# Performance work log

Measured on AMD Instinct MI355X. Metric: run time of the kernel, lower is better.

## Reference

```python
import jax, jax.numpy as jnp
import numpy as np

B, DIM, H, W = 2, 192, 256, 256
WIN = 4
EPS = 1e-5


def _cd_conj(x):
    if len(x) == 1:
        return x
    h = len(x) // 2
    return np.concatenate([_cd_conj(x[:h]), -x[h:]])


def _cd_mult(a, b):
    n = len(a)
    if n == 1:
        return a * b
    h = n // 2
    a1, a2, b1, b2 = a[:h], a[h:], b[:h], b[h:]
    c1 = _cd_mult(a1, b1) - _cd_mult(_cd_conj(b2), a2)
    c2 = _cd_mult(b2, a1) + _cd_mult(a2, _cd_conj(b1))
    return np.concatenate([c1, c2])


def _sedenion_table(n=16):
    # M[i, j, k] = sign s such that e_i * e_j = s * e_k (Cayley-Dickson)
    eye = np.eye(n, dtype=np.float32)
    M = np.zeros((n, n, n), dtype=np.float32)
    for i in range(n):
        for j in range(n):
            M[i, j] = _cd_mult(eye[i], eye[j])
    return M

SED_TABLE = jnp.asarray(_sedenion_table(16))  # (16,16,16)


def layer_norm(x, g, b):
    m = x.mean(-1, keepdims=True)
    v = ((x - m) ** 2).mean(-1, keepdims=True)
    return (x - m) * jax.lax.rsqrt(v + EPS) * g + b


def get_window(x):
    # (B,C,H,W) -> (B,H/4,W/4, s1*s2*C)
    b, c, h, w = x.shape
    x = x.reshape(b, c, h // WIN, WIN, w // WIN, WIN)
    x = x.transpose(0, 2, 4, 3, 5, 1)  # b, h', w', s1, s2, c
    return x.reshape(b, h // WIN, w // WIN, WIN * WIN * c)


def reverse_window(x, c):
    b, hh, ww, _ = x.shape
    x = x.reshape(b, hh, ww, WIN, WIN, c)
    x = x.transpose(0, 5, 1, 3, 2, 4)  # b, c, h', s1, w', s2
    return x.reshape(b, c, hh * WIN, ww * WIN)


def sedenion_full_weight(w_sed):
    # w_sed: (16, dim, dim) component weights -> (16*dim, 16*dim) structured matrix
    d = w_sed.shape[1]
    wf = jnp.einsum('ijk,jde->idke', SED_TABLE, w_sed)
    return wf.reshape(16 * d, 16 * w_sed.shape[2])


def setup_inputs() -> dict:
    key = jax.random.key(0)
    ks = jax.random.split(key, 8)
    d, dh = DIM, 4 * DIM
    s = 0.02
    return {
        'x': jax.random.normal(ks[0], (B, DIM, H, W), jnp.float32),
        'norm1_g': jnp.ones((d,), jnp.float32),
        'norm1_b': jnp.zeros((d,), jnp.float32),
        'w_sed': jax.random.normal(ks[1], (16, d, d), jnp.float32) * s,
        'proj_w': jax.random.normal(ks[2], (d, d), jnp.float32) * s,
        'proj_b': jnp.zeros((d,), jnp.float32),
        'norm2_g': jnp.ones((d,), jnp.float32),
        'norm2_b': jnp.zeros((d,), jnp.float32),
        'fc1_w': jax.random.normal(ks[3], (d, dh), jnp.float32) * s,
        'fc1_b': jnp.zeros((dh,), jnp.float32),
        'fc2_w': jax.random.normal(ks[4], (dh, d), jnp.float32) * s,
        'fc2_b': jnp.zeros((d,), jnp.float32),
    }


def reference(x, norm1_g, norm1_b, w_sed, proj_w, proj_b,
              norm2_g, norm2_b, fc1_w, fc1_b, fc2_w, fc2_b):
    b, c, h, w = x.shape
    # --- attention branch (norm1 -> window -> sedenion linear -> unwindow -> gelu -> proj) ---
    xn = layer_norm(x.transpose(0, 2, 3, 1), norm1_g, norm1_b).transpose(0, 3, 1, 2)
    xw = get_window(xn)                               # (B, H/4, W/4, 16*C)
    wf = sedenion_full_weight(w_sed)                  # (16C, 16C)
    xw = xw @ wf
    x1 = reverse_window(xw, c)                        # (B, C, H, W)
    y = x1.transpose(0, 2, 3, 1)                      # b h w c
    y = jax.nn.gelu(y, approximate=False)
    y = y @ proj_w + proj_b
    x = x + y.transpose(0, 3, 1, 2)
    # --- mlp branch ---
    hbr = layer_norm(x.transpose(0, 2, 3, 1), norm2_g, norm2_b)
    hbr = jax.nn.gelu(hbr @ fc1_w + fc1_b, approximate=False)
    hbr = hbr @ fc2_w + fc2_b
    x = x + hbr.transpose(0, 3, 1, 2)
    return x
```

## Files before the change

kernel.cpp:

```cpp
#include <hip/hip_runtime.h>

typedef short short8 __attribute__((ext_vector_type(8)));
typedef float f32x4 __attribute__((ext_vector_type(4)));

#define DEVINL __device__ __forceinline__

struct SedTab { signed char s[256]; unsigned char j[256]; };

static void cd_mult_host(const float* a, const float* b, float* r, int n) {
    if (n == 1) { r[0] = a[0] * b[0]; return; }
    int h = n / 2;
    float cb1[8], cb2[8], t1[8], t2[8], t3[8], t4[8];
    cb1[0] = b[0]; for (int i = 1; i < h; ++i) cb1[i] = -b[i];
    cb2[0] = b[h]; for (int i = 1; i < h; ++i) cb2[i] = -b[h + i];
    cd_mult_host(a,     b,   t1, h);
    cd_mult_host(cb2,   a+h, t2, h);
    cd_mult_host(b+h,   a,   t3, h);
    cd_mult_host(a+h,   cb1, t4, h);
    for (int i = 0; i < h; ++i) { r[i] = t1[i] - t2[i]; r[h + i] = t3[i] + t4[i]; }
}

static SedTab build_sed() {
    SedTab t{};
    for (int i = 0; i < 16; ++i)
        for (int jj = 0; jj < 16; ++jj) {
            float a[16] = {0}, b[16] = {0}, r[16] = {0};
            a[i] = 1.0f; b[jj] = 1.0f;
            cd_mult_host(a, b, r, 16);
            for (int k = 0; k < 16; ++k)
                if (r[k] != 0.0f) {
                    t.s[i * 16 + k] = (r[k] > 0.f) ? 1 : -1;
                    t.j[i * 16 + k] = (unsigned char)jj;
                }
        }
    return t;
}
static const SedTab g_sed = build_sed();

DEVINL unsigned short f2bf(float v) {
    union { float f; unsigned int u; } c; c.f = v;
    unsigned int r = (c.u + 0x7FFFu + ((c.u >> 16) & 1u)) >> 16;
    return (unsigned short)r;
}
DEVINL float bf2f(unsigned short u) {
    union { unsigned int i; float f; } c; c.i = ((unsigned int)u) << 16; return c.f;
}

DEVINL float gelu_f(float v) {
    float u = 1.5957691216f * (v + 0.044715f * v * v * v);
    return v / (1.0f + __expf(-u));
}

DEVINL void gl2lds16(const void* g, void* l) {
    __builtin_amdgcn_global_load_lds((__attribute__((address_space(1))) const unsigned int*)g,
                                     (__attribute__((address_space(3))) unsigned int*)l, 16, 0, 0);
}

DEVINL int swz(int k, int row) {
    return (k & ~63) | ((((k >> 3) ^ row) & 7) << 3) | (k & 7);
}

__global__ __launch_bounds__(256) void build_wft(const float* __restrict__ w_sed,
                                                 unsigned short* __restrict__ wfT,
                                                 SedTab tab) {
    __shared__ float t[32][33];
    int n0 = blockIdx.y * 32, kk0 = blockIdx.x * 32;
    int k = n0 / 192, i = kk0 / 192;
    int j = tab.j[i * 16 + k];
    float s = (float)tab.s[i * 16 + k];
    int e0 = n0 - k * 192, dd0 = kk0 - i * 192;
    int tx = threadIdx.x & 31, ty = threadIdx.x >> 5;
    const float* base = w_sed + ((size_t)j * 192 + dd0) * 192 + e0;
    for (int it = 0; it < 4; ++it) {
        int row = ty + it * 8;
        t[row][tx] = base[(size_t)row * 192 + tx];
    }
    __syncthreads();
    unsigned short* ob = wfT + (size_t)n0 * 3072 + kk0;
    for (int it = 0; it < 4; ++it) {
        int row = ty + it * 8;
        ob[(size_t)row * 3072 + tx] = f2bf(s * t[tx][row]);
    }
}

__global__ __launch_bounds__(256) void prep_w(const float* __restrict__ proj,
                                              const float* __restrict__ fc1,
                                              const float* __restrict__ fc2,
                                              unsigned short* __restrict__ projT,
                                              unsigned short* __restrict__ fc1T,
                                              unsigned short* __restrict__ fc2T) {
    int t = blockIdx.x * 256 + threadIdx.x;
    if (t < 192 * 192) projT[t] = f2bf(proj[(t % 192) * 192 + t / 192]);
    if (t < 768 * 192) {
        int n = t / 192, k = t % 192;
        fc1T[n * 192 + swz(k, n)] = f2bf(fc1[(size_t)k * 768 + n]);
    }
    if (t < 192 * 768) {
        int o = t / 768, k = t % 768;
        fc2T[o * 768 + swz(k, o)] = f2bf(fc2[(size_t)k * 192 + o]);
    }
}

__global__ __launch_bounds__(256) void ln1_win(const float* __restrict__ x,
                                               const float* __restrict__ g,
                                               const float* __restrict__ bta,
                                               unsigned short* __restrict__ xw,
                                               unsigned short* __restrict__ xwin) {
    __shared__ float vals[192 * 65];
    __shared__ float ps[8][64];
    __shared__ float mrs[2][64];
    int t = threadIdx.x;
    int bid = blockIdx.x;
    int x0 = (bid & 3) << 6;
    int y  = (bid >> 2) & 255;
    int b  = bid >> 10;
    int px = t & 63, cg = t >> 6;
    const float* xp = x + ((size_t)b * 192 * 65536) + (size_t)y * 256 + x0 + px;
    float s = 0.f, s2 = 0.f;
    for (int c = cg; c < 192; c += 4) {
        float v = xp[(size_t)c * 65536];
        vals[c * 65 + px] = v;
        s += v; s2 += v * v;
    }
    ps[cg][px] = s; ps[cg + 4][px] = s2;
    __syncthreads();
    if (t < 64) {
        float S  = ps[0][t] + ps[1][t] + ps[2][t] + ps[3][t];
        float S2 = ps[4][t] + ps[5][t] + ps[6][t] + ps[7][t];
        float mean = S * (1.0f / 192.0f);
        float var  = S2 * (1.0f / 192.0f) - mean * mean;
        mrs[0][t] = mean;
        mrs[1][t] = rsqrtf(var + 1e-5f);
    }
    __syncthreads();
    int wh = y >> 2, wr = y & 3;
    for (int i = t; i < 192 * 64; i += 256) {
        int p = i / 192;
        int c = i - p * 192;
        float v = vals[c * 65 + p];
        int xx = x0 + p;
        int ww = xx >> 2, wc = xx & 3;
        int gp = ((b * 64 + wh) * 64 + ww) * 16 + wr * 4 + wc;
        size_t o = (size_t)gp * 192 + c;
        xwin[o] = f2bf(v);
        xw[o] = f2bf((v - mrs[0][p]) * mrs[1][p] * g[c] + bta[c]);
    }
}

template<int TM, int TN, int EPI>
__global__ __launch_bounds__(256, 2) void gemm_bf16(
        const unsigned short* __restrict__ A, const unsigned short* __restrict__ BT,
        const float* __restrict__ bias, unsigned short* __restrict__ outB,
        unsigned short* __restrict__ xresb,
        const float* __restrict__ g2, const float* __restrict__ b2,
        int K, int N) {
    constexpr int WN = TN / 2;
    constexpr int NT = WN / 16;
    constexpr int MT = TM / 32;
    constexpr int HR = TM / 2;
    __shared__ __align__(16) char smem[(TM * 64 + TN * 64) * 2];
    short* lsA = (short*)smem;
    short* lsB = (short*)(smem + TM * 64 * 2);
    int tid = threadIdx.x, lane = tid & 63, wid = tid >> 6;
    int wrow = wid >> 1, wcol = wid & 1;
    int lm = lane & 15, lq = lane >> 4;
    int bm = blockIdx.x * TM, bn = blockIdx.y * TN;
    const unsigned short* Ag = A + (size_t)bm * K;
    const unsigned short* Bg = BT + (size_t)bn * K;
    f32x4 acc[MT][NT] = {};
    for (int k0 = 0; k0 < K; k0 += 64) {
        #pragma unroll
        for (int it = 0; it < TM / 32; ++it) {
            int p = (it * 4 + wid) * 64 + lane;
            int r = p >> 3;
            int q = (p & 7) ^ (r & 7);
            gl2lds16(Ag + (size_t)r * K + k0 + q * 8, lsA + (it * 4 + wid) * 512);
        }
        #pragma unroll
        for (int it = 0; it < TN / 32; ++it) {
            int p = (it * 4 + wid) * 64 + lane;
            int r = p >> 3;
            int q = (p & 7) ^ (r & 7);
            gl2lds16(Bg + (size_t)r * K + k0 + q * 8, lsB + (it * 4 + wid) * 512);
        }
        __syncthreads();
        #pragma unroll
        for (int s = 0; s < 2; ++s) {
            short8 af[MT], bfr[NT];
            #pragma unroll
            for (int mt = 0; mt < MT; ++mt) {
                int r = wrow * HR + mt * 16 + lm;
                int q = s * 4 + lq;
                int pos = r * 8 + (q ^ (r & 7));
                af[mt] = *(const short8*)&lsA[pos * 8];
            }
            #pragma unroll
            for (int nt = 0; nt < NT; ++nt) {
                int r = wcol * WN + nt * 16 + lm;
                int q = s * 4 + lq;
                int pos = r * 8 + (q ^ (r & 7));
                bfr[nt] = *(const short8*)&lsB[pos * 8];
            }
            #pragma unroll
            for (int mt = 0; mt < MT; ++mt)
                #pragma unroll
                for (int nt = 0; nt < NT; ++nt)
                    acc[mt][nt] = __builtin_amdgcn_mfma_f32_16x16x32_bf16(af[mt], bfr[nt], acc[mt][nt], 0, 0, 0);
        }
        __syncthreads();
    }
    int rowB = bm + wrow * HR + lq * 4;
    int colB = bn + wcol * WN + lm;

    if constexpr (EPI == 0) {
        #pragma unroll
        for (int mt = 0; mt < MT; ++mt)
            #pragma unroll
            for (int nt = 0; nt < NT; ++nt)
                #pragma unroll
                for (int r = 0; r < 4; ++r) {
                    int gr = rowB + mt * 16 + r;
                    int gc = colB + nt * 16;
                    float v = acc[mt][nt][r];
                    if (bias) v += bias[gc];
                    outB[(size_t)gr * N + gc] = f2bf(gelu_f(v));
                }
    } else {
        float sA[MT][4], s2A[MT][4];
        #pragma unroll
        for (int mt = 0; mt < MT; ++mt)
            #pragma unroll
            for (int r = 0; r < 4; ++r) { sA[mt][r] = 0.f; s2A[mt][r] = 0.f; }
        #pragma unroll
        for (int mt = 0; mt < MT; ++mt)
            #pragma unroll
            for (int nt = 0; nt < NT; ++nt)
                #pragma unroll
                for (int r = 0; r < 4; ++r) {
                    int gr = rowB + mt * 16 + r;
                    int gc = colB + nt * 16;
                    size_t o = (size_t)gr * 192 + gc;
                    float v = bf2f(xresb[o]) + acc[mt][nt][r] + bias[gc];
                    xresb[o] = f2bf(v);
                    acc[mt][nt][r] = v;
                    sA[mt][r] += v; s2A[mt][r] += v * v;
                }
        #pragma unroll
        for (int mt = 0; mt < MT; ++mt)
            #pragma unroll
            for (int r = 0; r < 4; ++r)
                #pragma unroll
                for (int msk = 1; msk < 16; msk <<= 1) {
                    sA[mt][r]  += __shfl_xor(sA[mt][r],  msk, 64);
                    s2A[mt][r] += __shfl_xor(s2A[mt][r], msk, 64);
                }
        float* psS   = (float*)smem;
        float* psS2  = psS + 256;
        float* pmean = psS2 + 256;
        float* prsig = pmean + 128;
        if (lm == 0) {
            #pragma unroll
            for (int mt = 0; mt < MT; ++mt)
                #pragma unroll
                for (int r = 0; r < 4; ++r) {
                    int rl = wrow * HR + mt * 16 + lq * 4 + r;
                    psS [rl * 2 + wcol] = sA[mt][r];
                    psS2[rl * 2 + wcol] = s2A[mt][r];
                }
        }
        __syncthreads();
        if (tid < TM) {
            float S  = psS[tid * 2]  + psS[tid * 2 + 1];
            float S2 = psS2[tid * 2] + psS2[tid * 2 + 1];
            float mean = S * (1.0f / 192.0f);
            float var  = S2 * (1.0f / 192.0f) - mean * mean;
            pmean[tid] = mean;
            prsig[tid] = rsqrtf(var + 1e-5f);
        }
        __syncthreads();
        float gw[NT], bw[NT];
        #pragma unroll
        for (int nt = 0; nt < NT; ++nt) {
            int gc = colB + nt * 16;
            gw[nt] = g2[gc]; bw[nt] = b2[gc];
        }
        #pragma unroll
        for (int mt = 0; mt < MT; ++mt)
            #pragma unroll
            for (int nt = 0; nt < NT; ++nt)
                #pragma unroll
                for (int r = 0; r < 4; ++r) {
                    int gr = rowB + mt * 16 + r;
                    int rl = wrow * HR + mt * 16 + lq * 4 + r;
                    int gc = colB + nt * 16;
                    float v = (acc[mt][nt][r] - pmean[rl]) * prsig[rl] * gw[nt] + bw[nt];
                    outB[(size_t)gr * 192 + swz(gc, gr)] = f2bf(v);
                }
    }
}

__global__ __launch_bounds__(256, 2) void ffn_fused(
        const unsigned short* __restrict__ A3, const unsigned short* __restrict__ fc1T,
        const unsigned short* __restrict__ fc2T, const float* __restrict__ b1,
        const float* __restrict__ b2, const unsigned short* __restrict__ xresb,
        float* __restrict__ outF) {
    __shared__ __align__(16) char smem[81920];
    short* wA0 = (short*)smem;
    short* wA1 = (short*)(smem + 24576);
    short* wB  = (short*)(smem + 49152);
    short* Sb  = (short*)(smem + 73728);
    int tid = threadIdx.x, lane = tid & 63, wid = tid >> 6;
    int wrow = wid >> 1, wcol = wid & 1;
    int lm = lane & 15, lq = lane >> 4;
    int bm = blockIdx.x * 64;

    const unsigned short* A3g = A3 + (size_t)bm * 192;

    auto stage_fc1 = [&](int slice, short* dst) {
        const unsigned short* f1g = fc1T + (size_t)slice * 64 * 192;
        #pragma unroll
        for (int it = 0; it < 6; ++it) {
            int ch = (it * 4 + wid) * 64 + lane;
            gl2lds16(f1g + ch * 8, dst + (it * 4 + wid) * 512);
        }
    };
    auto stage_fc2 = [&](int slice) {
        int kb = slice * 64;
        #pragma unroll
        for (int it = 0; it < 6; ++it) {
            int ch = (it * 4 + wid) * 64 + lane;
            gl2lds16(fc2T + (size_t)(ch >> 3) * 768 + kb + (ch & 7) * 8,
                     wB + (it * 4 + wid) * 512);
        }
    };

    stage_fc1(0, wA0);
    stage_fc1(1, wA1);
    stage_fc2(0);

    short8 af[6][2];
    #pragma unroll
    for (int ks = 0; ks < 6; ++ks) {
        int c = ks * 4 + lq;
        #pragma unroll
        for (int mt = 0; mt < 2; ++mt) {
            int r = wrow * 32 + mt * 16 + lm;
            int slot = (c & ~7) | ((c ^ r) & 7);
            af[ks][mt] = *(const short8*)&A3g[(size_t)r * 192 + slot * 8];
        }
    }
    __syncthreads();

    f32x4 acc2[2][6] = {};
    for (int nb = 0; nb < 12; ++nb) {
        const short* wAc = (nb & 1) ? wA1 : wA0;
        f32x4 acc1[2][2] = {};
        __builtin_amdgcn_s_setprio(1);
        #pragma unroll
        for (int ks = 0; ks < 6; ++ks) {
            int c = ks * 4 + lq;
            short8 bfr[2];
            #pragma unroll
            for (int nt = 0; nt < 2; ++nt) {
                int n = wcol * 32 + nt * 16 + lm;
                int slot = (c & ~7) | ((c ^ n) & 7);
                bfr[nt] = *(const short8*)&wAc[n * 192 + slot * 8];
            }
            #pragma unroll
            for (int mt = 0; mt < 2; ++mt)
                #pragma unroll
                for (int nt = 0; nt < 2; ++nt)
                    acc1[mt][nt] = __builtin_amdgcn_mfma_f32_16x16x32_bf16(af[ks][mt], bfr[nt], acc1[mt][nt], 0, 0, 0);
        }
        __builtin_amdgcn_s_setprio(0);
        #pragma unroll
        for (int nt = 0; nt < 2; ++nt) {
            int cl = wcol * 32 + nt * 16 + lm;
            float bv = b1[nb * 64 + cl];
            #pragma unroll
            for (int mt = 0; mt < 2; ++mt)
                #pragma unroll
                for (int r = 0; r < 4; ++r) {
                    int row = wrow * 32 + mt * 16 + lq * 4 + r;
                    float v = gelu_f(acc1[mt][nt][r] + bv);
                    int slot = ((cl >> 3) ^ row) & 7;
                    Sb[row * 64 + slot * 8 + (cl & 7)] = f2bf(v);
                }
        }
        asm volatile("s_waitcnt vmcnt(0) lgkmcnt(0)" ::: "memory");
        __builtin_amdgcn_sched_barrier(0);
        __builtin_amdgcn_s_barrier();
        __builtin_amdgcn_sched_barrier(0);
        if (nb < 10) stage_fc1(nb + 2, (nb & 1) ? wA1 : wA0);
        __builtin_amdgcn_s_setprio(1);
        #pragma unroll
        for (int ks = 0; ks < 2; ++ks) {
            int c = ks * 4 + lq;
            short8 sf[2], wf[6];
            #pragma unroll
            for (int mt = 0; mt < 2; ++mt) {
                int r = wrow * 32 + mt * 16 + lm;
                int slot = (c ^ r) & 7;
                sf[mt] = *(const short8*)&Sb[r * 64 + slot * 8];
            }
            #pragma unroll
            for (int nt = 0; nt < 6; ++nt) {
                int o = wcol * 96 + nt * 16 + lm;
                int slot = (c ^ o) & 7;
                wf[nt] = *(const short8*)&wB[o * 64 + slot * 8];
            }
            #pragma unroll
            for (int mt = 0; mt < 2; ++mt)
                #pragma unroll
                for (int nt = 0; nt < 6; ++nt)
                    acc2[mt][nt] = __builtin_amdgcn_mfma_f32_16x16x32_bf16(sf[mt], wf[nt], acc2[mt][nt], 0, 0, 0);
        }
        __builtin_amdgcn_s_setprio(0);
        asm volatile("s_waitcnt lgkmcnt(0)" ::: "memory");
        __builtin_amdgcn_sched_barrier(0);
        __builtin_amdgcn_s_barrier();
        __builtin_amdgcn_sched_barrier(0);
        if (nb < 11) stage_fc2(nb + 1);
    }
    float* T = (float*)smem;
    #pragma unroll
    for (int nt = 0; nt < 6; ++nt) {
        int col = wcol * 96 + nt * 16 + lm;
        float bv = b2[col];
        #pragma unroll
        for (int mt = 0; mt < 2; ++mt)
            #pragma unroll
            for (int r = 0; r < 4; ++r) {
                int row = wrow * 32 + mt * 16 + lq * 4 + r;
                float xr = bf2f(xresb[(size_t)(bm + row) * 192 + col]);
                T[row * 201 + col] = acc2[mt][nt][r] + bv + xr;
            }
    }
    __syncthreads();
    int b  = bm >> 16;
    int wh = (bm >> 10) & 63;
    int ww0 = (bm >> 4) & 63;
    int ybase = wh * 4, xbase = ww0 * 4;
    for (int idx = tid; idx < 3072; idx += 256) {
        int xq = idx & 3, run = idx >> 2;
        int c = run >> 2, wr = run & 3;
        int p = xq * 16 + wr * 4;
        f32x4 val;
        val[0] = T[(p + 0) * 201 + c];
        val[1] = T[(p + 1) * 201 + c];
        val[2] = T[(p + 2) * 201 + c];
        val[3] = T[(p + 3) * 201 + c];
        size_t o = (((size_t)b * 192 + c) * 256 + (ybase + wr)) * 256 + xbase + xq * 4;
        *(f32x4*)&outF[o] = val;
    }
}

extern "C" void kernel_launch(void* const* d_in, const int* in_sizes, int n_in,
                              void* d_out, int out_size, void* d_ws, size_t ws_size,
                              hipStream_t stream) {
    const float* x      = (const float*)d_in[0];
    const float* n1g    = (const float*)d_in[1];
    const float* n1b    = (const float*)d_in[2];
    const float* w_sed  = (const float*)d_in[3];
    const float* proj_w = (const float*)d_in[4];
    const float* proj_b = (const float*)d_in[5];
    const float* n2g    = (const float*)d_in[6];
    const float* n2b    = (const float*)d_in[7];
    const float* fc1_w  = (const float*)d_in[8];
    const float* fc1_b  = (const float*)d_in[9];
    const float* fc2_w  = (const float*)d_in[10];
    const float* fc2_b  = (const float*)d_in[11];
    float* out = (float*)d_out;

    char* ws = (char*)d_ws;
    unsigned short* wfT   = (unsigned short*)(ws);
    unsigned short* xw    = (unsigned short*)(ws + 18874368);
    unsigned short* A2    = (unsigned short*)(ws + 69206016);
    unsigned short* xresb = (unsigned short*)(ws + 119537664);
    unsigned short* projT = (unsigned short*)(ws + 169869312);
    unsigned short* fc1T  = (unsigned short*)(ws + 169943040);
    unsigned short* fc2T  = (unsigned short*)(ws + 170237952);
    unsigned short* A3    = A2;

    build_wft<<<dim3(96, 96), 256, 0, stream>>>(w_sed, wfT, g_sed);
    prep_w<<<576, 256, 0, stream>>>(proj_w, fc1_w, fc2_w, projT, fc1T, fc2T);
    ln1_win<<<2048, 256, 0, stream>>>(x, n1g, n1b, xw, xresb);

    gemm_bf16<128, 128, 0><<<dim3(64, 24), 256, 0, stream>>>(
        xw, wfT, nullptr, A2, nullptr, nullptr, nullptr, 3072, 3072);
    gemm_bf16<128, 192, 3><<<dim3(1024, 1), 256, 0, stream>>>(
        A2, projT, proj_b, A3, xresb, n2g, n2b, 192, 192);
    ffn_fused<<<2048, 256, 0, stream>>>(A3, fc1T, fc2T, fc1_b, fc2_b, xresb, out);
}
```

Before: 582.3 us.

## Enlarge fused FFN blocks to 256 rows and write output directly from registers

The fused FFN kernel now runs 1024-thread blocks covering 256 rows instead of 64, so each block stages the fc1/fc2 weight slices once for four times as many rows. Weight staging is rewritten as one or two 16-byte loads per thread. The LDS transpose epilogue is dropped: each lane adds bias and the bf16 residual and stores an f32x4 straight to NCHW output. GELU uses a hardware reciprocal instead of a divide. The risks are that __launch_bounds__(1024,4) caps registers per thread hard enough to cause spills, and the larger LDS footprint lowers occupancy.

New measurement: 832.2 us. +42.9%, slower.

```diff
diff --git a/kernel.cpp b/kernel.cpp
--- a/kernel.cpp
+++ b/kernel.cpp
@@ -48,7 +48,7 @@
 
 DEVINL float gelu_f(float v) {
     float u = 1.5957691216f * (v + 0.044715f * v * v * v);
-    return v / (1.0f + __expf(-u));
+    return v * __builtin_amdgcn_rcpf(1.0f + __expf(-u));
 }
 
 DEVINL void gl2lds16(const void* g, void* l) {
@@ -299,12 +299,12 @@
     }
 }
 
-__global__ __launch_bounds__(256, 2) void ffn_fused(
+__global__ __launch_bounds__(1024, 4) void ffn_fused(
         const unsigned short* __restrict__ A3, const unsigned short* __restrict__ fc1T,
         const unsigned short* __restrict__ fc2T, const float* __restrict__ b1,
         const float* __restrict__ b2, const unsigned short* __restrict__ xresb,
         float* __restrict__ outF) {
-    __shared__ __align__(16) char smem[81920];
+    __shared__ __align__(16) char smem[106496];
     short* wA0 = (short*)smem;
     short* wA1 = (short*)(smem + 24576);
     short* wB  = (short*)(smem + 49152);
@@ -312,25 +312,23 @@
     int tid = threadIdx.x, lane = tid & 63, wid = tid >> 6;
     int wrow = wid >> 1, wcol = wid & 1;
     int lm = lane & 15, lq = lane >> 4;
-    int bm = blockIdx.x * 64;
+    int bm = blockIdx.x * 256;
 
     const unsigned short* A3g = A3 + (size_t)bm * 192;
 
     auto stage_fc1 = [&](int slice, short* dst) {
         const unsigned short* f1g = fc1T + (size_t)slice * 64 * 192;
-        #pragma unroll
-        for (int it = 0; it < 6; ++it) {
-            int ch = (it * 4 + wid) * 64 + lane;
-            gl2lds16(f1g + ch * 8, dst + (it * 4 + wid) * 512);
-        }
+        gl2lds16(f1g + (size_t)tid * 8, dst + tid * 8);
+        if (tid < 512)
+            gl2lds16(f1g + (size_t)(1024 + tid) * 8, dst + (1024 + tid) * 8);
     };
     auto stage_fc2 = [&](int slice) {
         int kb = slice * 64;
-        #pragma unroll
-        for (int it = 0; it < 6; ++it) {
-            int ch = (it * 4 + wid) * 64 + lane;
-            gl2lds16(fc2T + (size_t)(ch >> 3) * 768 + kb + (ch & 7) * 8,
-                     wB + (it * 4 + wid) * 512);
+        int ch = tid;
+        gl2lds16(fc2T + (size_t)(ch >> 3) * 768 + kb + (ch & 7) * 8, wB + ch * 8);
+        if (tid < 512) {
+            int c2 = 1024 + tid;
+            gl2lds16(fc2T + (size_t)(c2 >> 3) * 768 + kb + (c2 & 7) * 8, wB + c2 * 8);
         }
     };
 
@@ -422,36 +420,26 @@
         __builtin_amdgcn_sched_barrier(0);
         if (nb < 11) stage_fc2(nb + 1);
     }
-    float* T = (float*)smem;
-    #pragma unroll
-    for (int nt = 0; nt < 6; ++nt) {
-        int col = wcol * 96 + nt * 16 + lm;
-        float bv = b2[col];
-        #pragma unroll
-        for (int mt = 0; mt < 2; ++mt)
-            #pragma unroll
-            for (int r = 0; r < 4; ++r) {
-                int row = wrow * 32 + mt * 16 + lq * 4 + r;
-                float xr = bf2f(xresb[(size_t)(bm + row) * 192 + col]);
-                T[row * 201 + col] = acc2[mt][nt][r] + bv + xr;
-            }
-    }
-    __syncthreads();
     int b  = bm >> 16;
     int wh = (bm >> 10) & 63;
     int ww0 = (bm >> 4) & 63;
     int ybase = wh * 4, xbase = ww0 * 4;
-    for (int idx = tid; idx < 3072; idx += 256) {
-        int xq = idx & 3, run = idx >> 2;
-        int c = run >> 2, wr = run & 3;
-        int p = xq * 16 + wr * 4;
-        f32x4 val;
-        val[0] = T[(p + 0) * 201 + c];
-        val[1] = T[(p + 1) * 201 + c];
-        val[2] = T[(p + 2) * 201 + c];
-        val[3] = T[(p + 3) * 201 + c];
-        size_t o = (((size_t)b * 192 + c) * 256 + (ybase + wr)) * 256 + xbase + xq * 4;
-        *(f32x4*)&outF[o] = val;
+    #pragma unroll
+    for (int nt = 0; nt < 6; ++nt) {
+        int c = wcol * 96 + nt * 16 + lm;
+        float bv = b2[c];
+        #pragma unroll
+        for (int mt = 0; mt < 2; ++mt) {
+            int p = wrow * 32 + mt * 16 + lq * 4;
+            f32x4 v;
+            #pragma unroll
+            for (int r = 0; r < 4; ++r)
+                v[r] = acc2[mt][nt][r] + bv + bf2f(xresb[(size_t)(bm + p + r) * 192 + c]);
+            int wr = lq;
+            int xq = wrow * 2 + mt;
+            size_t o = (((size_t)b * 192 + c) * 256 + (ybase + wr)) * 256 + xbase + xq * 4;
+            *(f32x4*)&outF[o] = v;
+        }
     }
 }
 
@@ -490,5 +478,5 @@
         xw, wfT, nullptr, A2, nullptr, nullptr, nullptr, 3072, 3072);
     gemm_bf16<128, 192, 3><<<dim3(1024, 1), 256, 0, stream>>>(
         A2, projT, proj_b, A3, xresb, n2g, n2b, 192, 192);
-    ffn_fused<<<2048, 256, 0, stream>>>(A3, fc1T, fc2T, fc1_b, fc2_b, xresb, out);
-}
+    ffn_fused<<<512, 1024, 0, stream>>>(A3, fc1T, fc2T, fc1_b, fc2_b, xresb, out);
+}
```

## Enlarge FFN block to 512 threads and single-buffer fc1 weights

Applied to the files above, without the earlier changes.

The fused FFN kernel now handles 128 rows per block with 8 waves instead of 64 rows with 4. The fc1 weight slice goes from double to single buffering, which cuts LDS to 64KB, and the epilogue writes its transpose in two 64-row passes so it fits in the smaller shared buffer. GELU uses a hardware reciprocal instead of a division. The aim is to share the weight tiles across more rows and raise occupancy. In exchange, fc1 loads are now exposed behind a vmcnt(0) wait, and the tighter launch bounds may force register spills given the large accumulator and fragment arrays.

Measured after the change: 797.7 us. +37.0%, slower.

```diff
diff --git a/kernel.cpp b/kernel.cpp
--- a/kernel.cpp
+++ b/kernel.cpp
@@ -48,7 +48,7 @@
 
 DEVINL float gelu_f(float v) {
     float u = 1.5957691216f * (v + 0.044715f * v * v * v);
-    return v / (1.0f + __expf(-u));
+    return v * __builtin_amdgcn_rcpf(1.0f + __expf(-u));
 }
 
 DEVINL void gl2lds16(const void* g, void* l) {
@@ -299,43 +299,41 @@
     }
 }
 
-__global__ __launch_bounds__(256, 2) void ffn_fused(
+__global__ __launch_bounds__(512, 4) void ffn_fused(
         const unsigned short* __restrict__ A3, const unsigned short* __restrict__ fc1T,
         const unsigned short* __restrict__ fc2T, const float* __restrict__ b1,
         const float* __restrict__ b2, const unsigned short* __restrict__ xresb,
         float* __restrict__ outF) {
-    __shared__ __align__(16) char smem[81920];
-    short* wA0 = (short*)smem;
-    short* wA1 = (short*)(smem + 24576);
-    short* wB  = (short*)(smem + 49152);
-    short* Sb  = (short*)(smem + 73728);
+    __shared__ __align__(16) char smem[65536];
+    short* wA = (short*)smem;
+    short* wB = (short*)(smem + 24576);
+    short* Sb = (short*)(smem + 49152);
     int tid = threadIdx.x, lane = tid & 63, wid = tid >> 6;
     int wrow = wid >> 1, wcol = wid & 1;
     int lm = lane & 15, lq = lane >> 4;
-    int bm = blockIdx.x * 64;
+    int bm = blockIdx.x * 128;
 
     const unsigned short* A3g = A3 + (size_t)bm * 192;
 
-    auto stage_fc1 = [&](int slice, short* dst) {
+    auto stage_fc1 = [&](int slice) {
         const unsigned short* f1g = fc1T + (size_t)slice * 64 * 192;
         #pragma unroll
-        for (int it = 0; it < 6; ++it) {
-            int ch = (it * 4 + wid) * 64 + lane;
-            gl2lds16(f1g + ch * 8, dst + (it * 4 + wid) * 512);
+        for (int it = 0; it < 3; ++it) {
+            int cb = it * 512 + wid * 64;
+            gl2lds16(f1g + (size_t)(cb + lane) * 8, wA + cb * 8);
         }
     };
     auto stage_fc2 = [&](int slice) {
         int kb = slice * 64;
         #pragma unroll
-        for (int it = 0; it < 6; ++it) {
-            int ch = (it * 4 + wid) * 64 + lane;
-            gl2lds16(fc2T + (size_t)(ch >> 3) * 768 + kb + (ch & 7) * 8,
-                     wB + (it * 4 + wid) * 512);
+        for (int it = 0; it < 3; ++it) {
+            int cb = it * 512 + wid * 64;
+            int ch = cb + lane;
+            gl2lds16(fc2T + (size_t)(ch >> 3) * 768 + kb + (ch & 7) * 8, wB + cb * 8);
         }
     };
 
-    stage_fc1(0, wA0);
-    stage_fc1(1, wA1);
+    stage_fc1(0);
     stage_fc2(0);
 
     short8 af[6][2];
@@ -353,7 +351,6 @@
 
     f32x4 acc2[2][6] = {};
     for (int nb = 0; nb < 12; ++nb) {
-        const short* wAc = (nb & 1) ? wA1 : wA0;
         f32x4 acc1[2][2] = {};
         __builtin_amdgcn_s_setprio(1);
         #pragma unroll
@@ -364,7 +361,7 @@
             for (int nt = 0; nt < 2; ++nt) {
                 int n = wcol * 32 + nt * 16 + lm;
                 int slot = (c & ~7) | ((c ^ n) & 7);
-                bfr[nt] = *(const short8*)&wAc[n * 192 + slot * 8];
+                bfr[nt] = *(const short8*)&wA[n * 192 + slot * 8];
             }
             #pragma unroll
             for (int mt = 0; mt < 2; ++mt)
@@ -391,7 +388,7 @@
         __builtin_amdgcn_sched_barrier(0);
         __builtin_amdgcn_s_barrier();
         __builtin_amdgcn_sched_barrier(0);
-        if (nb < 10) stage_fc1(nb + 2, (nb & 1) ? wA1 : wA0);
+        if (nb < 11) stage_fc1(nb + 1);
         __builtin_amdgcn_s_setprio(1);
         #pragma unroll
         for (int ks = 0; ks < 2; ++ks) {
@@ -416,7 +413,7 @@
                     acc2[mt][nt] = __builtin_amdgcn_mfma_f32_16x16x32_bf16(sf[mt], wf[nt], acc2[mt][nt], 0, 0, 0);
         }
         __builtin_amdgcn_s_setprio(0);
-        asm volatile("s_waitcnt lgkmcnt(0)" ::: "memory");
+        asm volatile("s_waitcnt vmcnt(0) lgkmcnt(0)" ::: "memory");
         __builtin_amdgcn_sched_barrier(0);
         __builtin_amdgcn_s_barrier();
         __builtin_amdgcn_sched_barrier(0);
@@ -424,34 +421,42 @@
     }
     float* T = (float*)smem;
     #pragma unroll
-    for (int nt = 0; nt < 6; ++nt) {
-        int col = wcol * 96 + nt * 16 + lm;
-        float bv = b2[col];
-        #pragma unroll
-        for (int mt = 0; mt < 2; ++mt)
-            #pragma unroll
-            for (int r = 0; r < 4; ++r) {
-                int row = wrow * 32 + mt * 16 + lq * 4 + r;
-                float xr = bf2f(xresb[(size_t)(bm + row) * 192 + col]);
-                T[row * 201 + col] = acc2[mt][nt][r] + bv + xr;
-            }
-    }
-    __syncthreads();
-    int b  = bm >> 16;
-    int wh = (bm >> 10) & 63;
-    int ww0 = (bm >> 4) & 63;
-    int ybase = wh * 4, xbase = ww0 * 4;
-    for (int idx = tid; idx < 3072; idx += 256) {
-        int xq = idx & 3, run = idx >> 2;
-        int c = run >> 2, wr = run & 3;
-        int p = xq * 16 + wr * 4;
-        f32x4 val;
-        val[0] = T[(p + 0) * 201 + c];
-        val[1] = T[(p + 1) * 201 + c];
-        val[2] = T[(p + 2) * 201 + c];
-        val[3] = T[(p + 3) * 201 + c];
-        size_t o = (((size_t)b * 192 + c) * 256 + (ybase + wr)) * 256 + xbase + xq * 4;
-        *(f32x4*)&outF[o] = val;
+    for (int pass = 0; pass < 2; ++pass) {
+        if ((wrow >> 1) == pass) {
+            #pragma unroll
+            for (int nt = 0; nt < 6; ++nt) {
+                int col = wcol * 96 + nt * 16 + lm;
+                float bv = b2[col];
+                #pragma unroll
+                for (int mt = 0; mt < 2; ++mt)
+                    #pragma unroll
+                    for (int r = 0; r < 4; ++r) {
+                        int row = wrow * 32 + mt * 16 + lq * 4 + r;
+                        int rowT = row - pass * 64;
+                        float xr = bf2f(xresb[(size_t)(bm + row) * 192 + col]);
+                        T[rowT * 201 + col] = acc2[mt][nt][r] + bv + xr;
+                    }
+            }
+        }
+        __syncthreads();
+        int bmg = bm + pass * 64;
+        int b  = bmg >> 16;
+        int wh = (bmg >> 10) & 63;
+        int ww0 = (bmg >> 4) & 63;
+        int ybase = wh * 4, xbase = ww0 * 4;
+        for (int idx = tid; idx < 3072; idx += 512) {
+            int xq = idx & 3, run = idx >> 2;
+            int c = run >> 2, wr = run & 3;
+            int p = xq * 16 + wr * 4;
+            f32x4 val;
+            val[0] = T[(p + 0) * 201 + c];
+            val[1] = T[(p + 1) * 201 + c];
+            val[2] = T[(p + 2) * 201 + c];
+            val[3] = T[(p + 3) * 201 + c];
+            size_t o = (((size_t)b * 192 + c) * 256 + (ybase + wr)) * 256 + xbase + xq * 4;
+            *(f32x4*)&outF[o] = val;
+        }
+        __syncthreads();
     }
 }
 
@@ -490,5 +495,5 @@
         xw, wfT, nullptr, A2, nullptr, nullptr, nullptr, 3072, 3072);
     gemm_bf16<128, 192, 3><<<dim3(1024, 1), 256, 0, stream>>>(
         A2, projT, proj_b, A3, xresb, n2g, n2b, 192, 192);
-    ffn_fused<<<2048, 256, 0, stream>>>(A3, fc1T, fc2T, fc1_b, fc2_b, xresb, out);
-}
+    ffn_fused<<<1024, 512, 0, stream>>>(A3, fc1T, fc2T, fc1_b, fc2_b, xresb, out);
+}
```
